# Performance work log

Measured on AMD Instinct MI355X. Metric: run time of the kernel, lower is better.

Reference implementation:

```python
import jax, jax.numpy as jnp
import numpy as np

N = 100000      # nodes
E = 3200000     # directed edges
F_IN = 128      # input node features
H = 16          # hidden width (fixed by module code)
C = 40          # classes
K_HOPS = 10
ALPHA = 0.1
BN_EPS = 1e-5


def gcn_conv(x, W, b, src, dst, n):
    """PyG GCNConv: add self-loops, symmetric D^-1/2 (A+I) D^-1/2 aggregation of x@W, plus bias."""
    loop = jnp.arange(n)
    s = jnp.concatenate([src, loop])
    d = jnp.concatenate([dst, loop])
    deg = jax.ops.segment_sum(jnp.ones(s.shape[0], x.dtype), d, num_segments=n)
    dinv = jnp.where(deg > 0, jax.lax.rsqrt(deg), 0.0)
    norm = dinv[s] * dinv[d]                      # [E+N]
    h = x @ W                                     # [N, out]
    out = jax.ops.segment_sum(h[s] * norm[:, None], d, num_segments=n)
    return out + b


def setup_inputs() -> dict:
    key = jax.random.key(0)
    ks = jax.random.split(key, 6)
    x = jax.random.normal(ks[0], (N, F_IN), jnp.float32)
    src = jax.random.randint(ks[1], (E,), 0, N)
    dst = jax.random.randint(ks[2], (E,), 0, N)
    glorot = lambda k, sh, fan: jax.random.normal(k, sh, jnp.float32) * np.float32(1.0 / np.sqrt(fan))
    W1 = glorot(ks[3], (F_IN, H), F_IN)
    b1 = jnp.zeros((H,), jnp.float32)
    gamma = jnp.ones((H,), jnp.float32)
    beta = jnp.zeros((H,), jnp.float32)
    Wl = glorot(ks[4], (H, H), H)
    bl = jnp.zeros((H,), jnp.float32)
    W2 = glorot(ks[5], (H, C), H)
    b2 = jnp.zeros((C,), jnp.float32)
    return dict(x=x, src=src, dst=dst, W1=W1, b1=b1, gamma=gamma, beta=beta,
                Wl=Wl, bl=bl, W2=W2, b2=b2)


def reference(x, src, dst, W1, b1, gamma, beta, Wl, bl, W2, b2):
    h = jax.nn.relu(gcn_conv(x, W1, b1, src, dst, N))
    # BatchNorm1d in training mode: biased batch statistics over nodes
    mean = h.mean(axis=0)
    var = h.var(axis=0)
    h = (h - mean) * jax.lax.rsqrt(var + BN_EPS) * gamma + beta
    # k_hops iterations of tiny linear-relu-residual blend
    def step(h, _):
        return ALPHA * jax.nn.relu(h @ Wl + bl) + (1.0 - ALPHA) * h, None
    h, _ = jax.lax.scan(step, h, None, length=K_HOPS)
    out = gcn_conv(h, W2, b2, src, dst, N)
    return jax.nn.log_softmax(out, axis=1)
```

## Files before the change

### kernel.cpp

```cpp
#include <hip/hip_runtime.h>
#include <hip/hip_fp16.h>
#include <math.h>

#define F_IN 128
#define H 16
#define C 40
#define K_HOPS 10
#define ALPHA 0.1f
#define BN_EPS 1e-5f

#define RB 256
#define RB_BITS 8
#define NBKT_MAX 512
#define SRC_MASK 0x1FFFF
#define PADQ 32
#define NDUMMY 2048
#define CAPB_BITS 14
#define CAPB (1 << CAPB_BITS)
#define STAGE_CAP 14336

typedef int v4i __attribute__((ext_vector_type(4)));

__global__ void k_zero(int* __restrict__ gcur, float* __restrict__ stats,
                       __half* __restrict__ h1h, __half* __restrict__ hh, int n) {
    int id = blockIdx.x * blockDim.x + threadIdx.x;
    if (id < NBKT_MAX) gcur[id] = id << CAPB_BITS;
    if (id < 32) stats[id] = 0.0f;
    int* z1 = (int*)(h1h + (size_t)n * H);
    int* z2 = (int*)(hh + (size_t)n * H);
    if (id < NDUMMY * H / 2) { z1[id] = 0; z2[id] = 0; }
}

#define BIN_CHUNK 4096
__global__ __launch_bounds__(512) void k_bin(const int* __restrict__ src,
                                             const int* __restrict__ dst,
                                             int* __restrict__ gcur,
                                             int* __restrict__ temp, int e) {
    __shared__ int hist[NBKT_MAX];
    __shared__ int cur[NBKT_MAX];
    __shared__ int gofs[NBKT_MAX];
    __shared__ int wsum[8];
    __shared__ int stageV[BIN_CHUNK];
    __shared__ int stageD[BIN_CHUNK];
    int t = threadIdx.x;
    hist[t] = 0;
    __syncthreads();
    int base = blockIdx.x * BIN_CHUNK;
    int cnt = e - base; if (cnt > BIN_CHUNK) cnt = BIN_CHUNK;
    const v4i* s4 = reinterpret_cast<const v4i*>(src + base);
    const v4i* d4 = reinterpret_cast<const v4i*>(dst + base);
    v4i sv[2], dv[2];
#pragma unroll
    for (int i = 0; i < 2; ++i) {
        int e0 = (t * 2 + i) * 4;
        if (e0 + 3 < cnt) { sv[i] = s4[t * 2 + i]; dv[i] = d4[t * 2 + i]; }
        else if (e0 < cnt) {
            int ts[4], td[4];
#pragma unroll
            for (int j = 0; j < 4; ++j) {
                int ei = e0 + j;
                ts[j] = (ei < cnt) ? src[base + ei] : 0;
                td[j] = (ei < cnt) ? dst[base + ei] : -1;
            }
            sv[i] = *reinterpret_cast<v4i*>(ts); dv[i] = *reinterpret_cast<v4i*>(td);
        } else { dv[i] = (v4i){-1, -1, -1, -1}; sv[i] = dv[i]; }
    }
#pragma unroll
    for (int i = 0; i < 2; ++i) {
        if (dv[i].x >= 0) atomicAdd(&hist[dv[i].x >> RB_BITS], 1);
        if (dv[i].y >= 0) atomicAdd(&hist[dv[i].y >> RB_BITS], 1);
        if (dv[i].z >= 0) atomicAdd(&hist[dv[i].z >> RB_BITS], 1);
        if (dv[i].w >= 0) atomicAdd(&hist[dv[i].w >> RB_BITS], 1);
    }
    __syncthreads();
    int v = hist[t];
    int lane = t & 63, wv = t >> 6;
    int s = v;
#pragma unroll
    for (int off = 1; off < 64; off <<= 1) { int u = __shfl_up(s, off); if (lane >= off) s += u; }
    if (lane == 63) wsum[wv] = s;
    __syncthreads();
    if (t < 8) {
        int x = wsum[t];
#pragma unroll
        for (int off = 1; off < 8; off <<= 1) { int u = __shfl_up(x, off); if (t >= off) x += u; }
        wsum[t] = x;
    }
    __syncthreads();
    int excl = s - v + (wv ? wsum[wv - 1] : 0);
    cur[t] = excl;
    int g = v ? atomicAdd(&gcur[t], v) : 0;
    gofs[t] = g - excl;
    __syncthreads();
#pragma unroll
    for (int i = 0; i < 2; ++i) {
        int ds[4] = { dv[i].x, dv[i].y, dv[i].z, dv[i].w };
        int ssx[4] = { sv[i].x, sv[i].y, sv[i].z, sv[i].w };
#pragma unroll
        for (int j = 0; j < 4; ++j) {
            int d = ds[j];
            if (d >= 0) {
                int b = d >> RB_BITS;
                int pos = atomicAdd(&cur[b], 1);
                stageV[pos] = ssx[j] | ((d & (RB - 1)) << 17);
                stageD[pos] = gofs[b];
            }
        }
    }
    __syncthreads();
    for (int i = t; i < cnt; i += 512)
        temp[stageD[i] + i] = stageV[i];
}

__global__ __launch_bounds__(256) void k_sort(const int* __restrict__ gcur,
                                              const int* __restrict__ temp,
                                              int* __restrict__ csr,
                                              int* __restrict__ ostart,
                                              int* __restrict__ oend,
                                              int* __restrict__ onode,
                                              float* __restrict__ dinv, int n) {
    __shared__ int hist[RB];
    __shared__ int cur[RB];
    __shared__ int wsum[8];
    __shared__ int qh[64];
    __shared__ int qb[64];
    __shared__ int ptotS;
    __shared__ int stage[STAGE_CAP];
    int t = threadIdx.x;
    int bkt = blockIdx.x;
    int start = bkt << CAPB_BITS;
    int endi = gcur[bkt];
    int nv = endi - start;
    int n4 = nv >> 2;
    const v4i* t4 = reinterpret_cast<const v4i*>(temp + start);
    hist[t] = 0;
    if (t < 64) qh[t] = 0;
    __syncthreads();
    for (int k = t; k < n4; k += 256) {
        v4i v = t4[k];
        atomicAdd(&hist[v.x >> 17], 1);
        atomicAdd(&hist[v.y >> 17], 1);
        atomicAdd(&hist[v.z >> 17], 1);
        atomicAdd(&hist[v.w >> 17], 1);
    }
    for (int k = start + (n4 << 2) + t; k < endi; k += 256)
        atomicAdd(&hist[temp[k] >> 17], 1);
    __syncthreads();
    int node = (bkt << RB_BITS) + t;
    int h = hist[t];
    int p = (h + PADQ - 1) & ~(PADQ - 1);
    bool va = (node < n);
    if (va) dinv[node] = rsqrtf((float)(h + 1));
    int lane = t & 63, wv = t >> 6;
    int s = p;
#pragma unroll
    for (int off = 1; off < 64; off <<= 1) { int u = __shfl_up(s, off); if (lane >= off) s += u; }
    if (lane == 63) wsum[wv] = s;
    __syncthreads();
    if (t < 4) {
        int x = wsum[t];
#pragma unroll
        for (int off = 1; off < 4; off <<= 1) { int u = __shfl_up(x, off); if (t >= off) x += u; }
        wsum[t] = x;
        if (t == 3) ptotS = x;
    }
    __syncthreads();
    int pexcl = s - p + (wv ? wsum[wv - 1] : 0);
    int s0 = start + pexcl;
    int q = 63 - min(p >> 5, 63);
    int r = atomicAdd(&qh[q], 1);
    __syncthreads();
    int ptotal = ptotS;
    if (t == 0) {
        int run = 0;
        for (int i = 0; i < 64; ++i) { qb[i] = run; run += qh[i]; }
    }
    __syncthreads();
    int ga = (bkt << RB_BITS) + qb[q] + r;
    ostart[ga] = s0; oend[ga] = s0 + p; onode[ga] = va ? node : -1;

    if (ptotal <= STAGE_CAP) {
        cur[t] = pexcl;
        for (int i = t; i < ptotal; i += 256) stage[i] = -1;
        __syncthreads();
        for (int k = t; k < n4; k += 256) {
            v4i v = t4[k];
            int p0 = atomicAdd(&cur[v.x >> 17], 1); stage[p0] = v.x & SRC_MASK;
            int p1 = atomicAdd(&cur[v.y >> 17], 1); stage[p1] = v.y & SRC_MASK;
            int p2 = atomicAdd(&cur[v.z >> 17], 1); stage[p2] = v.z & SRC_MASK;
            int p3 = atomicAdd(&cur[v.w >> 17], 1); stage[p3] = v.w & SRC_MASK;
        }
        for (int k = start + (n4 << 2) + t; k < endi; k += 256) {
            int v = temp[k];
            int pos = atomicAdd(&cur[v >> 17], 1);
            stage[pos] = v & SRC_MASK;
        }
        __syncthreads();
        for (int i = t * 4; i < ptotal; i += 1024) {
            v4i v = *reinterpret_cast<const v4i*>(&stage[i]);
            int gi = start + i;
            v.x = (v.x < 0) ? n + ((gi + 0) & (NDUMMY - 1)) : v.x;
            v.y = (v.y < 0) ? n + ((gi + 1) & (NDUMMY - 1)) : v.y;
            v.z = (v.z < 0) ? n + ((gi + 2) & (NDUMMY - 1)) : v.z;
            v.w = (v.w < 0) ? n + ((gi + 3) & (NDUMMY - 1)) : v.w;
            *reinterpret_cast<v4i*>(&csr[gi]) = v;
        }
    } else {
        cur[t] = s0;
        __syncthreads();
        for (int k = start + t; k < endi; k += 256) {
            int v = temp[k];
            int pos = atomicAdd(&cur[v >> 17], 1);
            csr[pos] = v & SRC_MASK;
        }
        __syncthreads();
        for (int i = s0 + h; i < s0 + p; ++i) csr[i] = n + (i & (NDUMMY - 1));
    }
}

__global__ __launch_bounds__(256) void k_mm1(const float* __restrict__ x,
                                             const float* __restrict__ W1,
                                             const float* __restrict__ dinv,
                                             __half* __restrict__ h1h, int n) {
    __shared__ __align__(16) float xs[16 * 132];
    __shared__ __align__(16) float ws[128 * 16];
    int t = threadIdx.x;
    int node0 = blockIdx.x * 16;
    const float4* x4 = reinterpret_cast<const float4*>(x);
    const float4* w4 = reinterpret_cast<const float4*>(W1);
#pragma unroll
    for (int r = 0; r < 2; ++r) {
        int f = t + r * 256;
        int nl = f >> 5, k4 = f & 31;
        int nn = node0 + nl; if (nn >= n) nn = n - 1;
        *reinterpret_cast<float4*>(&xs[nl * 132 + k4 * 4]) = x4[(size_t)nn * 32 + k4];
        *reinterpret_cast<float4*>(&ws[f * 4]) = w4[f];
    }
    __syncthreads();
    int nl = t >> 4, j = t & 15;
    float acc = 0.0f;
#pragma unroll 8
    for (int k = 0; k < 128; ++k)
        acc = fmaf(xs[nl * 132 + k], ws[k * 16 + j], acc);
    int node = node0 + nl;
    if (node < n) h1h[(size_t)node * H + j] = __float2half(acc * dinv[node]);
}

__device__ __forceinline__ void acc8(float* a, int4 gv) {
    const __half2* h = reinterpret_cast<const __half2*>(&gv);
    float2 f0 = __half22float2(h[0]);
    float2 f1 = __half22float2(h[1]);
    float2 f2 = __half22float2(h[2]);
    float2 f3 = __half22float2(h[3]);
    a[0] += f0.x; a[1] += f0.y; a[2] += f1.x; a[3] += f1.y;
    a[4] += f2.x; a[5] += f2.y; a[6] += f3.x; a[7] += f3.y;
}

__global__ __launch_bounds__(256) void k_gather1(const int* __restrict__ ostart,
                                                 const int* __restrict__ oend,
                                                 const int* __restrict__ onode,
                                                 const int* __restrict__ csr,
                                                 const __half* __restrict__ h1h,
                                                 const float* __restrict__ dinv,
                                                 const float* __restrict__ b1,
                                                 float* __restrict__ hout,
                                                 float* __restrict__ stats, int n) {
    __shared__ float sm[32];
    __shared__ float b1s[16];
    int t = threadIdx.x;
    if (t < 32) sm[t] = 0.0f;
    if (t < 16) b1s[t] = b1[t];
    __syncthreads();
    int idx = blockIdx.x * 256 + t;
    int g = idx >> 2;
    int L = idx & 3, p = L >> 1, jj = L & 1;
    int node = __builtin_nontemporal_load(onode + g);
    float a[8];
#pragma unroll
    for (int k = 0; k < 8; ++k) a[k] = 0.0f;
    const int4* tab = reinterpret_cast<const int4*>(h1h);
    if (node >= 0) {
        int c  = (__builtin_nontemporal_load(ostart + g) >> 2) + (p << 2);
        int ce = __builtin_nontemporal_load(oend + g) >> 2;
        const v4i* csr4 = reinterpret_cast<const v4i*>(csr);
        for (; c < ce; c += 8) {
            v4i e0 = __builtin_nontemporal_load(csr4 + c);
            v4i e1 = __builtin_nontemporal_load(csr4 + c + 1);
            v4i e2 = __builtin_nontemporal_load(csr4 + c + 2);
            v4i e3 = __builtin_nontemporal_load(csr4 + c + 3);
            int4 g0  = tab[(size_t)e0.x * 2 + jj];
            int4 g1  = tab[(size_t)e0.y * 2 + jj];
            int4 g2  = tab[(size_t)e0.z * 2 + jj];
            int4 g3  = tab[(size_t)e0.w * 2 + jj];
            int4 g4  = tab[(size_t)e1.x * 2 + jj];
            int4 g5  = tab[(size_t)e1.y * 2 + jj];
            int4 g6  = tab[(size_t)e1.z * 2 + jj];
            int4 g7  = tab[(size_t)e1.w * 2 + jj];
            int4 g8  = tab[(size_t)e2.x * 2 + jj];
            int4 g9  = tab[(size_t)e2.y * 2 + jj];
            int4 g10 = tab[(size_t)e2.z * 2 + jj];
            int4 g11 = tab[(size_t)e2.w * 2 + jj];
            int4 g12 = tab[(size_t)e3.x * 2 + jj];
            int4 g13 = tab[(size_t)e3.y * 2 + jj];
            int4 g14 = tab[(size_t)e3.z * 2 + jj];
            int4 g15 = tab[(size_t)e3.w * 2 + jj];
            acc8(a, g0);  acc8(a, g1);  acc8(a, g2);  acc8(a, g3);
            acc8(a, g4);  acc8(a, g5);  acc8(a, g6);  acc8(a, g7);
            acc8(a, g8);  acc8(a, g9);  acc8(a, g10); acc8(a, g11);
            acc8(a, g12); acc8(a, g13); acc8(a, g14); acc8(a, g15);
        }
    }
#pragma unroll
    for (int k = 0; k < 8; ++k) a[k] += __shfl_xor(a[k], 2);
    float din = 0.0f;
    int4 sv = make_int4(0, 0, 0, 0);
    if (node >= 0) {
        din = dinv[node];
        sv = tab[(size_t)node * 2 + jj];
    }
    float v[8];
    {
        const __half2* h = reinterpret_cast<const __half2*>(&sv);
        float2 f0 = __half22float2(h[0]), f1 = __half22float2(h[1]);
        float2 f2 = __half22float2(h[2]), f3 = __half22float2(h[3]);
        float s8[8] = { f0.x, f0.y, f1.x, f1.y, f2.x, f2.y, f3.x, f3.y };
        bool writer = (node >= 0) && (p == 0);
#pragma unroll
        for (int k = 0; k < 8; ++k) {
            float val = fmaxf(din * (a[k] + s8[k]) + b1s[jj * 8 + k], 0.0f);
            v[k] = writer ? val : 0.0f;
        }
        if (writer) {
            float4* o = reinterpret_cast<float4*>(hout + (size_t)node * H + jj * 8);
            o[0] = make_float4(v[0], v[1], v[2], v[3]);
            o[1] = make_float4(v[4], v[5], v[6], v[7]);
        }
    }
#pragma unroll
    for (int k = 0; k < 8; ++k) {
        float s1 = v[k], s2 = v[k] * v[k];
        s1 += __shfl_xor(s1, 2);  s2 += __shfl_xor(s2, 2);
        s1 += __shfl_xor(s1, 4);  s2 += __shfl_xor(s2, 4);
        s1 += __shfl_xor(s1, 8);  s2 += __shfl_xor(s2, 8);
        s1 += __shfl_xor(s1, 16); s2 += __shfl_xor(s2, 16);
        s1 += __shfl_xor(s1, 32); s2 += __shfl_xor(s2, 32);
        if ((t & 63) < 2) {
            atomicAdd(&sm[jj * 8 + k], s1);
            atomicAdd(&sm[16 + jj * 8 + k], s2);
        }
    }
    __syncthreads();
    if (t < 32) atomicAdd(&stats[t], sm[t]);
}

__global__ void k_bncoef(float* __restrict__ stats, const float* __restrict__ gamma,
                         const float* __restrict__ beta, float nf) {
    int j = threadIdx.x;
    if (j < 16) {
        float mean = stats[j] / nf;
        float var = stats[16 + j] / nf - mean * mean;
        float a = gamma[j] * rsqrtf(var + BN_EPS);
        float c = beta[j] - mean * a;
        stats[j] = a;
        stats[16 + j] = c;
    }
}

__global__ __launch_bounds__(256) void k_hops(const float* __restrict__ h,
                                              __half* __restrict__ hh,
                                              const float* __restrict__ stats,
                                              const float* __restrict__ Wl,
                                              const float* __restrict__ bl,
                                              const float* __restrict__ dinv, int n) {
    __shared__ float wl[256], bls[16], av[16], cv[16];
    int t = threadIdx.x;
    wl[t] = Wl[(t & 15) * 16 + (t >> 4)];
    if (t < 16) { bls[t] = bl[t]; av[t] = stats[t]; cv[t] = stats[16 + t]; }
    __syncthreads();
    int node = blockIdx.x * 256 + t;
    if (node >= n) return;
    float hr[16];
    {
        const float4* hp = reinterpret_cast<const float4*>(h + (size_t)node * H);
        float4 v0 = hp[0], v1 = hp[1], v2 = hp[2], v3 = hp[3];
        hr[0] = v0.x; hr[1] = v0.y; hr[2] = v0.z; hr[3] = v0.w;
        hr[4] = v1.x; hr[5] = v1.y; hr[6] = v1.z; hr[7] = v1.w;
        hr[8] = v2.x; hr[9] = v2.y; hr[10] = v2.z; hr[11] = v2.w;
        hr[12] = v3.x; hr[13] = v3.y; hr[14] = v3.z; hr[15] = v3.w;
    }
#pragma unroll
    for (int j = 0; j < 16; ++j) hr[j] = hr[j] * av[j] + cv[j];
    for (int it = 0; it < K_HOPS; ++it) {
        float tmp[16];
#pragma unroll
        for (int j = 0; j < 16; ++j) {
            float a = bls[j];
#pragma unroll
            for (int k = 0; k < 16; ++k) a = fmaf(hr[k], wl[j * 16 + k], a);
            tmp[j] = fmaxf(a, 0.0f);
        }
#pragma unroll
        for (int j = 0; j < 16; ++j) hr[j] = ALPHA * tmp[j] + (1.0f - ALPHA) * hr[j];
    }
    {
        float din = dinv[node];
        __half2 ph[8];
#pragma unroll
        for (int i = 0; i < 8; ++i)
            ph[i] = __floats2half2_rn(hr[2 * i] * din, hr[2 * i + 1] * din);
        int4* hp = reinterpret_cast<int4*>(hh + (size_t)node * H);
        hp[0] = *reinterpret_cast<int4*>(&ph[0]);
        hp[1] = *reinterpret_cast<int4*>(&ph[4]);
    }
}

__global__ __launch_bounds__(256) void k_gather2(const int* __restrict__ ostart,
                                                 const int* __restrict__ oend,
                                                 const int* __restrict__ onode,
                                                 const int* __restrict__ csr,
                                                 const __half* __restrict__ hh,
                                                 const float* __restrict__ dinv,
                                                 float* __restrict__ agg, int n) {
    int t = threadIdx.x;
    int idx = blockIdx.x * 256 + t;
    int g = idx >> 2;
    int L = idx & 3, p = L >> 1, jj = L & 1;
    int node = __builtin_nontemporal_load(onode + g);
    float a[8];
#pragma unroll
    for (int k = 0; k < 8; ++k) a[k] = 0.0f;
    const int4* tab = reinterpret_cast<const int4*>(hh);
    if (node >= 0) {
        int c  = (__builtin_nontemporal_load(ostart + g) >> 2) + (p << 2);
        int ce = __builtin_nontemporal_load(oend + g) >> 2;
        const v4i* csr4 = reinterpret_cast<const v4i*>(csr);
        for (; c < ce; c += 8) {
            v4i e0 = __builtin_nontemporal_load(csr4 + c);
            v4i e1 = __builtin_nontemporal_load(csr4 + c + 1);
            v4i e2 = __builtin_nontemporal_load(csr4 + c + 2);
            v4i e3 = __builtin_nontemporal_load(csr4 + c + 3);
            int4 g0  = tab[(size_t)e0.x * 2 + jj];
            int4 g1  = tab[(size_t)e0.y * 2 + jj];
            int4 g2  = tab[(size_t)e0.z * 2 + jj];
            int4 g3  = tab[(size_t)e0.w * 2 + jj];
            int4 g4  = tab[(size_t)e1.x * 2 + jj];
            int4 g5  = tab[(size_t)e1.y * 2 + jj];
            int4 g6  = tab[(size_t)e1.z * 2 + jj];
            int4 g7  = tab[(size_t)e1.w * 2 + jj];
            int4 g8  = tab[(size_t)e2.x * 2 + jj];
            int4 g9  = tab[(size_t)e2.y * 2 + jj];
            int4 g10 = tab[(size_t)e2.z * 2 + jj];
            int4 g11 = tab[(size_t)e2.w * 2 + jj];
            int4 g12 = tab[(size_t)e3.x * 2 + jj];
            int4 g13 = tab[(size_t)e3.y * 2 + jj];
            int4 g14 = tab[(size_t)e3.z * 2 + jj];
            int4 g15 = tab[(size_t)e3.w * 2 + jj];
            acc8(a, g0);  acc8(a, g1);  acc8(a, g2);  acc8(a, g3);
            acc8(a, g4);  acc8(a, g5);  acc8(a, g6);  acc8(a, g7);
            acc8(a, g8);  acc8(a, g9);  acc8(a, g10); acc8(a, g11);
            acc8(a, g12); acc8(a, g13); acc8(a, g14); acc8(a, g15);
        }
    }
#pragma unroll
    for (int k = 0; k < 8; ++k) a[k] += __shfl_xor(a[k], 2);
    if (node >= 0 && p == 0) {
        float din = dinv[node];
        int4 sv = tab[(size_t)node * 2 + jj];
        const __half2* h = reinterpret_cast<const __half2*>(&sv);
        float2 f0 = __half22float2(h[0]), f1 = __half22float2(h[1]);
        float2 f2 = __half22float2(h[2]), f3 = __half22float2(h[3]);
        float s8[8] = { f0.x, f0.y, f1.x, f1.y, f2.x, f2.y, f3.x, f3.y };
        float v[8];
#pragma unroll
        for (int k = 0; k < 8; ++k) v[k] = din * (a[k] + s8[k]);
        float4* o = reinterpret_cast<float4*>(agg + (size_t)node * H + jj * 8);
        o[0] = make_float4(v[0], v[1], v[2], v[3]);
        o[1] = make_float4(v[4], v[5], v[6], v[7]);
    }
}

__global__ __launch_bounds__(256) void k_final(const float* __restrict__ agg2,
                                               const float* __restrict__ W2,
                                               const float* __restrict__ b2,
                                               float* __restrict__ out, int n) {
    __shared__ float w2s[16 * 40];
    __shared__ float b2s[40];
    __shared__ float ostage[40 * 257];
    int t = threadIdx.x;
    for (int i = t; i < 640; i += 256) w2s[i] = W2[i];
    if (t < 40) b2s[t] = b2[t];
    __syncthreads();
    int node = blockIdx.x * 256 + t;
    if (node < n) {
        float g[16];
        const float4* ap = reinterpret_cast<const float4*>(agg2 + (size_t)node * H);
#pragma unroll
        for (int r = 0; r < 4; ++r) {
            float4 a = ap[r];
            g[r * 4 + 0] = a.x; g[r * 4 + 1] = a.y; g[r * 4 + 2] = a.z; g[r * 4 + 3] = a.w;
        }
        float z[40];
#pragma unroll
        for (int j = 0; j < 40; ++j) {
            float a = b2s[j];
#pragma unroll
            for (int k = 0; k < 16; ++k) a = fmaf(g[k], w2s[k * 40 + j], a);
            z[j] = a;
        }
        float m = z[0];
#pragma unroll
        for (int j = 1; j < 40; ++j) m = fmaxf(m, z[j]);
        float s = 0.0f;
#pragma unroll
        for (int j = 0; j < 40; ++j) s += expf(z[j] - m);
        float lse = m + logf(s);
#pragma unroll
        for (int j = 0; j < 40; ++j) ostage[j * 257 + t] = z[j] - lse;
    }
    __syncthreads();
    int nodes = n - blockIdx.x * 256;
    if (nodes > 256) nodes = 256;
    int total = nodes * 40;
    size_t base = (size_t)blockIdx.x * 256 * 40;
    for (int i = t; i < total; i += 256) {
        int nl = i / 40;
        int j = i - nl * 40;
        out[base + i] = ostage[j * 257 + nl];
    }
}

extern "C" void kernel_launch(void* const* d_in, const int* in_sizes, int n_in,
                              void* d_out, int out_size, void* d_ws, size_t ws_size,
                              hipStream_t stream) {
    const float* x     = (const float*)d_in[0];
    const int*   src   = (const int*)d_in[1];
    const int*   dst   = (const int*)d_in[2];
    const float* W1    = (const float*)d_in[3];
    const float* b1    = (const float*)d_in[4];
    const float* gamma = (const float*)d_in[5];
    const float* beta  = (const float*)d_in[6];
    const float* Wl    = (const float*)d_in[7];
    const float* bl    = (const float*)d_in[8];
    const float* W2    = (const float*)d_in[9];
    const float* b2    = (const float*)d_in[10];
    float* out = (float*)d_out;

    int n = in_sizes[0] / F_IN;
    int e = in_sizes[1];
    int nbkt = (n + RB - 1) >> RB_BITS;
    int nAlign = (n + 15) & ~15;
    int nG = nbkt * RB;
    size_t bktB = (size_t)nbkt << CAPB_BITS;
    size_t hTileB = (size_t)nAlign * H * 4;
    size_t unionB = bktB * 4;
    if (unionB < 2 * hTileB) unionB = 2 * hTileB;

    char* wsb = (char*)d_ws;
    int*    csr      = (int*)wsb;      wsb += (bktB + 64) * 4;
    char*   uni      = wsb;            wsb += unionB;
    int*    temp     = (int*)uni;
    float*  hbuf     = (float*)uni;
    float*  agg2     = (float*)(uni + hTileB);
    int*    ostart   = (int*)wsb;      wsb += (size_t)(nG + 16) * 4;
    int*    oend     = (int*)wsb;      wsb += (size_t)(nG + 16) * 4;
    int*    onode    = (int*)wsb;      wsb += (size_t)(nG + 16) * 4;
    float*  dinv     = (float*)wsb;    wsb += (size_t)nAlign * 4;
    int*    gcur     = (int*)wsb;      wsb += NBKT_MAX * 4;
    float*  stats    = (float*)wsb;    wsb += 64 * 4;
    __half* h1h      = (__half*)wsb;   wsb += (size_t)(nAlign + NDUMMY + 16) * H * 2;
    __half* hh       = (__half*)wsb;   wsb += (size_t)(nAlign + NDUMMY + 16) * H * 2;

    k_zero<<<64, 256, 0, stream>>>(gcur, stats, h1h, hh, n);
    k_bin<<<(e + BIN_CHUNK - 1) / BIN_CHUNK, 512, 0, stream>>>(src, dst, gcur, temp, e);
    k_sort<<<nbkt, 256, 0, stream>>>(gcur, temp, csr, ostart, oend, onode, dinv, n);
    k_mm1<<<(n + 15) / 16, 256, 0, stream>>>(x, W1, dinv, h1h, n);
    k_gather1<<<nbkt * 4, 256, 0, stream>>>(ostart, oend, onode, csr, h1h, dinv, b1, hbuf, stats, n);
    k_bncoef<<<1, 16, 0, stream>>>(stats, gamma, beta, (float)n);
    k_hops<<<(n + 255) / 256, 256, 0, stream>>>(hbuf, hh, stats, Wl, bl, dinv, n);
    k_gather2<<<nbkt * 4, 256, 0, stream>>>(ostart, oend, onode, csr, hh, dinv, agg2, n);
    k_final<<<(n + 255) / 256, 256, 0, stream>>>(agg2, W2, b2, out, n);
}
```

Before: 267.8 us.

## Fuse BN coefficient computation into hops and final projection into second gather

Removes the single-thread-block BN coefficient kernel by having every hops block recompute the 16 scale/shift values from the stats. Fuses the final W2 projection plus log-softmax into the second gather kernel: aggregated features are staged in shared memory, and four threads per node each compute 10 classes, combining max and sum across lanes with shuffles. This removes two launches and the agg2 round trip through global memory. The cost is extra shared memory and register pressure in the gather kernel, and output writes that are less coalesced since they follow the gather's node order.

New measurement: 266.0 us. No clear change (-0.7%).

```diff
diff --git a/kernel.cpp b/kernel.cpp
--- a/kernel.cpp
+++ b/kernel.cpp
@@ -353,29 +353,25 @@
     if (t < 32) atomicAdd(&stats[t], sm[t]);
 }
 
-__global__ void k_bncoef(float* __restrict__ stats, const float* __restrict__ gamma,
-                         const float* __restrict__ beta, float nf) {
-    int j = threadIdx.x;
-    if (j < 16) {
-        float mean = stats[j] / nf;
-        float var = stats[16 + j] / nf - mean * mean;
-        float a = gamma[j] * rsqrtf(var + BN_EPS);
-        float c = beta[j] - mean * a;
-        stats[j] = a;
-        stats[16 + j] = c;
-    }
-}
-
 __global__ __launch_bounds__(256) void k_hops(const float* __restrict__ h,
                                               __half* __restrict__ hh,
                                               const float* __restrict__ stats,
+                                              const float* __restrict__ gamma,
+                                              const float* __restrict__ beta,
                                               const float* __restrict__ Wl,
                                               const float* __restrict__ bl,
-                                              const float* __restrict__ dinv, int n) {
+                                              const float* __restrict__ dinv, int n, float nf) {
     __shared__ float wl[256], bls[16], av[16], cv[16];
     int t = threadIdx.x;
     wl[t] = Wl[(t & 15) * 16 + (t >> 4)];
-    if (t < 16) { bls[t] = bl[t]; av[t] = stats[t]; cv[t] = stats[16 + t]; }
+    if (t < 16) {
+        bls[t] = bl[t];
+        float mean = stats[t] / nf;
+        float var = stats[16 + t] / nf - mean * mean;
+        float aa = gamma[t] * rsqrtf(var + BN_EPS);
+        av[t] = aa;
+        cv[t] = beta[t] - mean * aa;
+    }
     __syncthreads();
     int node = blockIdx.x * 256 + t;
     if (node >= n) return;
@@ -414,14 +410,21 @@
     }
 }
 
-__global__ __launch_bounds__(256) void k_gather2(const int* __restrict__ ostart,
-                                                 const int* __restrict__ oend,
-                                                 const int* __restrict__ onode,
-                                                 const int* __restrict__ csr,
-                                                 const __half* __restrict__ hh,
-                                                 const float* __restrict__ dinv,
-                                                 float* __restrict__ agg, int n) {
+__global__ __launch_bounds__(256) void k_g2f(const int* __restrict__ ostart,
+                                             const int* __restrict__ oend,
+                                             const int* __restrict__ onode,
+                                             const int* __restrict__ csr,
+                                             const __half* __restrict__ hh,
+                                             const float* __restrict__ dinv,
+                                             const float* __restrict__ W2,
+                                             const float* __restrict__ b2,
+                                             float* __restrict__ out, int n) {
+    __shared__ __align__(16) float w2t[40 * 20];
+    __shared__ float b2s[40];
+    __shared__ __align__(16) float feat[64 * 20];
     int t = threadIdx.x;
+    for (int i = t; i < 640; i += 256) w2t[(i >> 4) * 20 + (i & 15)] = W2[(i & 15) * 40 + (i >> 4)];
+    if (t < 40) b2s[t] = b2[t];
     int idx = blockIdx.x * 256 + t;
     int g = idx >> 2;
     int L = idx & 3, p = L >> 1, jj = L & 1;
@@ -463,6 +466,7 @@
     }
 #pragma unroll
     for (int k = 0; k < 8; ++k) a[k] += __shfl_xor(a[k], 2);
+    int nl = t >> 2;
     if (node >= 0 && p == 0) {
         float din = dinv[node];
         int4 sv = tab[(size_t)node * 2 + jj];
@@ -473,59 +477,47 @@
         float v[8];
 #pragma unroll
         for (int k = 0; k < 8; ++k) v[k] = din * (a[k] + s8[k]);
-        float4* o = reinterpret_cast<float4*>(agg + (size_t)node * H + jj * 8);
-        o[0] = make_float4(v[0], v[1], v[2], v[3]);
-        o[1] = make_float4(v[4], v[5], v[6], v[7]);
-    }
-}
-
-__global__ __launch_bounds__(256) void k_final(const float* __restrict__ agg2,
-                                               const float* __restrict__ W2,
-                                               const float* __restrict__ b2,
-                                               float* __restrict__ out, int n) {
-    __shared__ float w2s[16 * 40];
-    __shared__ float b2s[40];
-    __shared__ float ostage[40 * 257];
-    int t = threadIdx.x;
-    for (int i = t; i < 640; i += 256) w2s[i] = W2[i];
-    if (t < 40) b2s[t] = b2[t];
-    __syncthreads();
-    int node = blockIdx.x * 256 + t;
-    if (node < n) {
-        float g[16];
-        const float4* ap = reinterpret_cast<const float4*>(agg2 + (size_t)node * H);
-#pragma unroll
-        for (int r = 0; r < 4; ++r) {
-            float4 a = ap[r];
-            g[r * 4 + 0] = a.x; g[r * 4 + 1] = a.y; g[r * 4 + 2] = a.z; g[r * 4 + 3] = a.w;
-        }
-        float z[40];
-#pragma unroll
-        for (int j = 0; j < 40; ++j) {
-            float a = b2s[j];
-#pragma unroll
-            for (int k = 0; k < 16; ++k) a = fmaf(g[k], w2s[k * 40 + j], a);
-            z[j] = a;
-        }
-        float m = z[0];
-#pragma unroll
-        for (int j = 1; j < 40; ++j) m = fmaxf(m, z[j]);
-        float s = 0.0f;
-#pragma unroll
-        for (int j = 0; j < 40; ++j) s += expf(z[j] - m);
-        float lse = m + logf(s);
-#pragma unroll
-        for (int j = 0; j < 40; ++j) ostage[j * 257 + t] = z[j] - lse;
-    }
-    __syncthreads();
-    int nodes = n - blockIdx.x * 256;
-    if (nodes > 256) nodes = 256;
-    int total = nodes * 40;
-    size_t base = (size_t)blockIdx.x * 256 * 40;
-    for (int i = t; i < total; i += 256) {
-        int nl = i / 40;
-        int j = i - nl * 40;
-        out[base + i] = ostage[j * 257 + nl];
+        *reinterpret_cast<float4*>(&feat[nl * 20 + jj * 8])     = make_float4(v[0], v[1], v[2], v[3]);
+        *reinterpret_cast<float4*>(&feat[nl * 20 + jj * 8 + 4]) = make_float4(v[4], v[5], v[6], v[7]);
+    }
+    __syncthreads();
+    float4 f0 = *reinterpret_cast<const float4*>(&feat[nl * 20]);
+    float4 f1 = *reinterpret_cast<const float4*>(&feat[nl * 20 + 4]);
+    float4 f2 = *reinterpret_cast<const float4*>(&feat[nl * 20 + 8]);
+    float4 f3 = *reinterpret_cast<const float4*>(&feat[nl * 20 + 12]);
+    int cb = (t & 3) * 10;
+    float z[10];
+#pragma unroll
+    for (int j = 0; j < 10; ++j) {
+        const float4* wr = reinterpret_cast<const float4*>(&w2t[(cb + j) * 20]);
+        float4 w0 = wr[0], w1 = wr[1], w2v = wr[2], w3 = wr[3];
+        float acc = b2s[cb + j];
+        acc = fmaf(f0.x, w0.x, acc); acc = fmaf(f0.y, w0.y, acc);
+        acc = fmaf(f0.z, w0.z, acc); acc = fmaf(f0.w, w0.w, acc);
+        acc = fmaf(f1.x, w1.x, acc); acc = fmaf(f1.y, w1.y, acc);
+        acc = fmaf(f1.z, w1.z, acc); acc = fmaf(f1.w, w1.w, acc);
+        acc = fmaf(f2.x, w2v.x, acc); acc = fmaf(f2.y, w2v.y, acc);
+        acc = fmaf(f2.z, w2v.z, acc); acc = fmaf(f2.w, w2v.w, acc);
+        acc = fmaf(f3.x, w3.x, acc); acc = fmaf(f3.y, w3.y, acc);
+        acc = fmaf(f3.z, w3.z, acc); acc = fmaf(f3.w, w3.w, acc);
+        z[j] = acc;
+    }
+    float m = z[0];
+#pragma unroll
+    for (int j = 1; j < 10; ++j) m = fmaxf(m, z[j]);
+    m = fmaxf(m, __shfl_xor(m, 1));
+    m = fmaxf(m, __shfl_xor(m, 2));
+    float s = 0.0f;
+#pragma unroll
+    for (int j = 0; j < 10; ++j) s += expf(z[j] - m);
+    s += __shfl_xor(s, 1);
+    s += __shfl_xor(s, 2);
+    float lse = m + logf(s);
+    if (node >= 0) {
+        float2* o = reinterpret_cast<float2*>(out + (size_t)node * 40 + cb);
+#pragma unroll
+        for (int j = 0; j < 5; ++j)
+            o[j] = make_float2(z[2 * j] - lse, z[2 * j + 1] - lse);
     }
 }
 
@@ -553,14 +545,13 @@
     size_t bktB = (size_t)nbkt << CAPB_BITS;
     size_t hTileB = (size_t)nAlign * H * 4;
     size_t unionB = bktB * 4;
-    if (unionB < 2 * hTileB) unionB = 2 * hTileB;
+    if (unionB < hTileB) unionB = hTileB;
 
     char* wsb = (char*)d_ws;
     int*    csr      = (int*)wsb;      wsb += (bktB + 64) * 4;
     char*   uni      = wsb;            wsb += unionB;
     int*    temp     = (int*)uni;
     float*  hbuf     = (float*)uni;
-    float*  agg2     = (float*)(uni + hTileB);
     int*    ostart   = (int*)wsb;      wsb += (size_t)(nG + 16) * 4;
     int*    oend     = (int*)wsb;      wsb += (size_t)(nG + 16) * 4;
     int*    onode    = (int*)wsb;      wsb += (size_t)(nG + 16) * 4;
@@ -575,8 +566,6 @@
     k_sort<<<nbkt, 256, 0, stream>>>(gcur, temp, csr, ostart, oend, onode, dinv, n);
     k_mm1<<<(n + 15) / 16, 256, 0, stream>>>(x, W1, dinv, h1h, n);
     k_gather1<<<nbkt * 4, 256, 0, stream>>>(ostart, oend, onode, csr, h1h, dinv, b1, hbuf, stats, n);
-    k_bncoef<<<1, 16, 0, stream>>>(stats, gamma, beta, (float)n);
-    k_hops<<<(n + 255) / 256, 256, 0, stream>>>(hbuf, hh, stats, Wl, bl, dinv, n);
-    k_gather2<<<nbkt * 4, 256, 0, stream>>>(ostart, oend, onode, csr, hh, dinv, agg2, n);
-    k_final<<<(n + 255) / 256, 256, 0, stream>>>(agg2, W2, b2, out, n);
-}
+    k_hops<<<(n + 255) / 256, 256, 0, stream>>>(hbuf, hh, stats, gamma, beta, Wl, bl, dinv, n, (float)n);
+    k_g2f<<<nbkt * 4, 256, 0, stream>>>(ostart, oend, onode, csr, hh, dinv, W2, b2, out, n);
+}
```
